# Kernel tuning notes

Measured on AMD Instinct MI355X. Metric: run time of the kernel, lower is better.

## Reference

```python
import jax, jax.numpy as jnp
import numpy as np

V = 50000
E = 300000
B = 4
LAT = 512
H = 128
L = 3


def setup_inputs() -> dict:
    key = jax.random.key(0)
    ks = jax.random.split(key, 8)
    vertex_xyz = jax.random.normal(ks[0], (V, 3), jnp.float32)
    latent = jax.random.normal(ks[1], (B, LAT), jnp.float32)
    edge_index = jax.random.randint(ks[2], (2, E), 0, V, dtype=jnp.int32)
    def lin(k, out_f, in_f):
        return jax.random.normal(k, (out_f, in_f), jnp.float32) / np.float32(np.sqrt(in_f))
    W_in = lin(ks[3], H, LAT + 3)
    b_in = jnp.zeros((H,), jnp.float32)
    conv_W = jax.random.normal(ks[4], (L, H, H), jnp.float32) / np.float32(np.sqrt(H))
    conv_b = jnp.zeros((L, H), jnp.float32)
    W_out = lin(ks[5], 3, H)
    b_out = jnp.zeros((3,), jnp.float32)
    return dict(vertex_xyz=vertex_xyz, latent=latent, edge_index=edge_index,
                W_in=W_in, b_in=b_in, conv_W=conv_W, conv_b=conv_b,
                W_out=W_out, b_out=b_out)


def _edge_norm(edge_index, B_, V_):
    """GCN symmetric normalization for edge_index tiled B times (same node ids,
    as in the original code's edge_index.repeat(1, B)) plus self-loops on all
    N = B*V flattened nodes. Structure is identical across layers, so compute once."""
    N = B_ * V_
    ei = jnp.tile(edge_index, (1, B_))                 # (2, E*B), ids in [0, V)
    loops = jnp.arange(N, dtype=edge_index.dtype)
    row = jnp.concatenate([ei[0], loops])              # source
    col = jnp.concatenate([ei[1], loops])              # target
    deg = jax.ops.segment_sum(jnp.ones(row.shape, jnp.float32), col, num_segments=N)
    dis = jnp.where(deg > 0, jax.lax.rsqrt(jnp.maximum(deg, 1.0)), 0.0)
    norm = dis[row] * dis[col]                         # (E*B + N,)
    return row, col, norm, N


def reference(vertex_xyz, latent, edge_index, W_in, b_in, conv_W, conv_b, W_out, b_out):
    B_, V_ = latent.shape[0], vertex_xyz.shape[0]
    row, col, norm, N = _edge_norm(edge_index, B_, V_)

    # concat template xyz with broadcast latent -> (B*V, LAT+3)
    x = jnp.concatenate([
        jnp.broadcast_to(vertex_xyz[None], (B_, V_, 3)),
        jnp.broadcast_to(latent[:, None, :], (B_, V_, latent.shape[-1])),
    ], axis=-1).reshape(B_ * V_, -1)

    x = jax.nn.relu(x @ W_in.T + b_in)                 # (N, H)

    for l in range(conv_W.shape[0]):
        h = x @ conv_W[l].T                            # linear (no bias before aggregation)
        agg = jax.ops.segment_sum(norm[:, None] * h[row], col, num_segments=N)
        x = jax.nn.relu(agg + conv_b[l])

    out = x @ W_out.T + b_out                          # (N, 3)
    return out.reshape(B_, V_, 3)
```

## Files before the change

### kernel.cpp

```cpp
#include <hip/hip_runtime.h>
#include <hip/hip_bf16.h>

typedef __attribute__((ext_vector_type(8))) short short8;
typedef __attribute__((ext_vector_type(4))) float f32x4;

#define V_ 50000
#define E_ 300000
#define B_ 4
#define LAT_ 512
#define H_ 128
#define L_ 3
#define N_ (B_*V_)

#define SCAN_B 512
#define SCAN_G ((V_ + SCAN_B - 1) / SCAN_B)

__device__ inline void bsplit(float v, ushort& hi, ushort& lo) {
    __hip_bfloat16 hb = __float2bfloat16(v);
    float hf = __bfloat162float(hb);
    __hip_bfloat16 lb = __float2bfloat16(v - hf);
    hi = *(ushort*)&hb; lo = *(ushort*)&lb;
}
__device__ inline float bjoin(ushort h, ushort l) {
    __hip_bfloat16 hb = *(__hip_bfloat16*)&h;
    __hip_bfloat16 lb = *(__hip_bfloat16*)&l;
    return __bfloat162float(hb) + __bfloat162float(lb);
}


__global__ void k_zero(int* __restrict__ deg, int* __restrict__ cursor) {
    int i = blockIdx.x * 256 + threadIdx.x;
    if (i < V_) { deg[i] = 0; cursor[i] = 0; }
}

__global__ void k_deg(const int* __restrict__ dst, int* __restrict__ deg) {
    int e = blockIdx.x * 256 + threadIdx.x;
    if (e < E_) atomicAdd(&deg[dst[e]], 1);
}

__global__ __launch_bounds__(SCAN_B) void k_scan1(const int* __restrict__ deg,
                                                  int* __restrict__ off,
                                                  float* __restrict__ dis,
                                                  int* __restrict__ part) {
    int t = threadIdx.x;
    int i = blockIdx.x * SCAN_B + t;
    int d = (i < V_) ? deg[i] : 0;
    __shared__ int sm[SCAN_B];
    sm[t] = d;
    __syncthreads();
    int val = d;
    for (int s = 1; s < SCAN_B; s <<= 1) {
        int o = (t >= s) ? sm[t - s] : 0;
        __syncthreads();
        val += o;
        sm[t] = val;
        __syncthreads();
    }
    if (i < V_) {
        off[i] = val - d;
        dis[i] = rsqrtf((float)(B_ * d + 1));
    }
    if (t == SCAN_B - 1) part[blockIdx.x] = val;
}

__global__ void k_scan2(int* __restrict__ part) {
    __shared__ int sm[128];
    int t = threadIdx.x;
    int v = (t < SCAN_G) ? part[t] : 0;
    sm[t] = v;
    __syncthreads();
    int val = v;
    for (int s = 1; s < 128; s <<= 1) {
        int o = (t >= s) ? sm[t - s] : 0;
        __syncthreads();
        val += o;
        sm[t] = val;
        __syncthreads();
    }
    if (t < SCAN_G) part[t] = val - v;
}

__global__ __launch_bounds__(SCAN_B) void k_scan3(int* __restrict__ off,
                                                  const int* __restrict__ part) {
    int i = blockIdx.x * SCAN_B + threadIdx.x;
    if (i < V_) off[i] += part[blockIdx.x];
    if (i == 0) off[V_] = E_;
}

__global__ void k_fill(const int* __restrict__ src, const int* __restrict__ dst,
                       const int* __restrict__ off, int* __restrict__ cursor,
                       int* __restrict__ csr) {
    int e = blockIdx.x * 256 + threadIdx.x;
    if (e < E_) {
        int c = dst[e];
        int p = atomicAdd(&cursor[c], 1);
        csr[off[c] + p] = src[e];
    }
}


__global__ void k_wsplit(const float* __restrict__ W, ushort* __restrict__ Whi,
                         ushort* __restrict__ Wlo) {
    int i = blockIdx.x * 256 + threadIdx.x;
    float w = W[i];
    ushort hi, lo; bsplit(w, hi, lo);
    Whi[i] = hi; Wlo[i] = lo;
}

__global__ void k_latproj(const float* __restrict__ Win, const float* __restrict__ bin,
                          const float* __restrict__ latent, float* __restrict__ latproj) {
    int t = blockIdx.x * 128 + threadIdx.x;
    if (t >= B_ * H_) return;
    int b = t >> 7, j = t & 127;
    const float* wr = Win + (size_t)j * (LAT_ + 3) + 3;
    const float* lp = latent + (size_t)b * LAT_;
    float s = bin[j];
    for (int k = 0; k < LAT_; k++) s = fmaf(wr[k], lp[k], s);
    latproj[t] = s;
}


__global__ __launch_bounds__(512, 4) void k_big(
        const float* __restrict__ xyz, const float* __restrict__ latproj,
        const float* __restrict__ Win,
        const ushort* __restrict__ Whi, const ushort* __restrict__ Wlo,
        const float* __restrict__ convb,
        const float* __restrict__ Wout, const float* __restrict__ bout,
        float* __restrict__ out) {
    __shared__ __align__(16) char smem[65536];
    const int tid = threadIdx.x;
    const int row0 = V_ + blockIdx.x * 64;
    const int lane = tid & 63;
    const int wid  = tid >> 6;
    const int l15  = lane & 15;
    const int kg   = lane >> 4;
    const int n0   = wid * 16;
    const int tr   = tid >> 4;
    const int c0   = (tid & 15) * 8;

#pragma unroll
    for (int rep = 0; rep < 2; rep++) {
        int row = tr + rep * 32;
        int node = row0 + row;
        ushort hs[8], ls[8];
        if (node < N_) {
            int v = node % V_, b = node / V_;
            float xv0 = xyz[v*3+0], xv1 = xyz[v*3+1], xv2 = xyz[v*3+2];
#pragma unroll
            for (int i = 0; i < 8; i++) {
                int j = c0 + i;
                float s = latproj[b*H_ + j];
                s = fmaf(Win[(size_t)j*(LAT_+3)+0], xv0, s);
                s = fmaf(Win[(size_t)j*(LAT_+3)+1], xv1, s);
                s = fmaf(Win[(size_t)j*(LAT_+3)+2], xv2, s);
                s = fmaxf(s, 0.f);
                bsplit(s, hs[i], ls[i]);
            }
        } else {
#pragma unroll
            for (int i = 0; i < 8; i++) { hs[i] = 0; ls[i] = 0; }
        }
        int bo = (c0*2) ^ ((row & 7) << 4);
        *(uint4*)(smem + row*256 + bo) = *(uint4*)hs;
        *(uint4*)(smem + 16384 + row*256 + bo) = *(uint4*)ls;
    }
    __syncthreads();

    int cur = 0;
    for (int l = 0; l < L_; l++) {
        const ushort* Whp = Whi + (size_t)l*H_*H_;
        const ushort* Wlp = Wlo + (size_t)l*H_*H_;
        short8 wh[4], wl[4];
#pragma unroll
        for (int ks = 0; ks < 4; ks++) {
            const ushort* bh = Whp + (size_t)(n0 + l15)*H_ + ks*32 + kg*4;
            const ushort* bl = Wlp + (size_t)(n0 + l15)*H_ + ks*32 + kg*4;
            union { short8 v; uint2 u[2]; } uh, ul;
            uh.u[0] = *(const uint2*)bh;  uh.u[1] = *(const uint2*)(bh + 16);
            ul.u[0] = *(const uint2*)bl;  ul.u[1] = *(const uint2*)(bl + 16);
            wh[ks] = uh.v; wl[ks] = ul.v;
        }
        const char* sb = smem + cur*32768;
        f32x4 acc[4];
#pragma unroll
        for (int mt = 0; mt < 4; mt++) acc[mt] = (f32x4){0.f,0.f,0.f,0.f};
#pragma unroll
        for (int mt = 0; mt < 4; mt++) {
            int row = mt*16 + l15;
            int swz = (row & 7) << 4;
            const char* rbh = sb + row*256;
            const char* rbl = sb + 16384 + row*256;
#pragma unroll
            for (int ks = 0; ks < 4; ks++) {
                int cc = ks*64 + kg*8;
                union { short8 v; uint2 u[2]; } ah, al;
                ah.u[0] = *(const uint2*)(rbh + (cc ^ swz));
                ah.u[1] = *(const uint2*)(rbh + ((cc+32) ^ swz));
                al.u[0] = *(const uint2*)(rbl + (cc ^ swz));
                al.u[1] = *(const uint2*)(rbl + ((cc+32) ^ swz));
                acc[mt] = __builtin_amdgcn_mfma_f32_16x16x32_bf16(ah.v, wh[ks], acc[mt], 0,0,0);
                acc[mt] = __builtin_amdgcn_mfma_f32_16x16x32_bf16(al.v, wh[ks], acc[mt], 0,0,0);
                acc[mt] = __builtin_amdgcn_mfma_f32_16x16x32_bf16(ah.v, wl[ks], acc[mt], 0,0,0);
            }
        }
        __syncthreads();
        char* db = smem + (cur^1)*32768;
        float bv = convb[l*H_ + n0 + l15];
        int bo = (n0 + l15) * 2;
#pragma unroll
        for (int mt = 0; mt < 4; mt++)
#pragma unroll
            for (int j = 0; j < 4; j++) {
                int row = mt*16 + kg*4 + j;
                int swz = (row & 7) << 4;
                float v = fmaxf(acc[mt][j] + bv, 0.f);
                ushort hi, lo; bsplit(v, hi, lo);
                *(ushort*)(db + row*256 + (bo ^ swz)) = hi;
                *(ushort*)(db + 16384 + row*256 + (bo ^ swz)) = lo;
            }
        __syncthreads();
        cur ^= 1;
    }

    const char* ob = smem + cur*32768;
    float wo0[8], wo1[8], wo2[8];
#pragma unroll
    for (int i = 0; i < 8; i++) {
        wo0[i] = Wout[0*H_ + c0 + i];
        wo1[i] = Wout[1*H_ + c0 + i];
        wo2[i] = Wout[2*H_ + c0 + i];
    }
#pragma unroll
    for (int rep = 0; rep < 2; rep++) {
        int row = tr + rep*32;
        int node = row0 + row;
        int bo = (c0*2) ^ ((row & 7) << 4);
        uint4 uh = *(const uint4*)(ob + row*256 + bo);
        uint4 ul = *(const uint4*)(ob + 16384 + row*256 + bo);
        const ushort* hp = (const ushort*)&uh;
        const ushort* lp = (const ushort*)&ul;
        float p0 = 0.f, p1 = 0.f, p2 = 0.f;
#pragma unroll
        for (int i = 0; i < 8; i++) {
            float xv = bjoin(hp[i], lp[i]);
            p0 = fmaf(xv, wo0[i], p0);
            p1 = fmaf(xv, wo1[i], p1);
            p2 = fmaf(xv, wo2[i], p2);
        }
#pragma unroll
        for (int m = 1; m < 16; m <<= 1) {
            p0 += __shfl_xor(p0, m);
            p1 += __shfl_xor(p1, m);
            p2 += __shfl_xor(p2, m);
        }
        if ((tid & 15) == 0 && node < N_) {
            out[(size_t)node*3 + 0] = p0 + bout[0];
            out[(size_t)node*3 + 1] = p1 + bout[1];
            out[(size_t)node*3 + 2] = p2 + bout[2];
        }
    }
}


template<int MODE>
__global__ __launch_bounds__(256, 4) void k_layerb0(
        const ushort* __restrict__ xh, const ushort* __restrict__ xl,
        const float* __restrict__ xyz, const float* __restrict__ latproj,
        const float* __restrict__ Win,
        const ushort* __restrict__ Whp, const ushort* __restrict__ Wlp,
        float* __restrict__ h) {
    __shared__ __align__(16) char smem[16896];
    const int tid = threadIdx.x;
    const int row0 = blockIdx.x * 32;
    const int lane = tid & 63;
    const int wid  = tid >> 6;
    const int l15  = lane & 15;
    const int kg   = lane >> 4;
    const int n0   = wid * 32;
    const int tr   = tid >> 4;
    const int c0   = (tid & 15) * 8;

    if (MODE == 0) {
#pragma unroll
        for (int rep = 0; rep < 2; rep++) {
            int row = tr + rep * 16;
            int v = row0 + row;
            ushort hs[8], ls[8];
            if (v < V_) {
                float xv0 = xyz[v*3+0], xv1 = xyz[v*3+1], xv2 = xyz[v*3+2];
#pragma unroll
                for (int i = 0; i < 8; i++) {
                    int j = c0 + i;
                    float s = latproj[j];
                    s = fmaf(Win[(size_t)j*(LAT_+3)+0], xv0, s);
                    s = fmaf(Win[(size_t)j*(LAT_+3)+1], xv1, s);
                    s = fmaf(Win[(size_t)j*(LAT_+3)+2], xv2, s);
                    s = fmaxf(s, 0.f);
                    bsplit(s, hs[i], ls[i]);
                }
            } else {
#pragma unroll
                for (int i = 0; i < 8; i++) { hs[i] = 0; ls[i] = 0; }
            }
            int bo = (c0*2) ^ ((row & 7) << 4);
            *(uint4*)(smem + row*256 + bo) = *(uint4*)hs;
            *(uint4*)(smem + 8192 + row*256 + bo) = *(uint4*)ls;
        }
    } else {
#pragma unroll
        for (int k = 0; k < 4; k++) {
            int chunk = tid + k*256;
            int p  = chunk >> 9;
            int r  = (chunk >> 4) & 31;
            int cb = (chunk & 15) * 16;
            int grow = row0 + r;
            uint4 g = {0u,0u,0u,0u};
            if (grow < V_)
                g = *(const uint4*)((const char*)((p ? xl : xh) + (size_t)grow*H_) + cb);
            *(uint4*)(smem + p*8192 + r*256 + (cb ^ ((r & 7) << 4))) = g;
        }
    }
    __syncthreads();

    short8 wh[2][4], wl[2][4];
#pragma unroll
    for (int nt = 0; nt < 2; nt++)
#pragma unroll
        for (int ks = 0; ks < 4; ks++) {
            const ushort* bh = Whp + (size_t)(n0 + nt*16 + l15)*H_ + ks*32 + kg*4;
            const ushort* bl = Wlp + (size_t)(n0 + nt*16 + l15)*H_ + ks*32 + kg*4;
            union { short8 v; uint2 u[2]; } uh, ul;
            uh.u[0] = *(const uint2*)bh;  uh.u[1] = *(const uint2*)(bh + 16);
            ul.u[0] = *(const uint2*)bl;  ul.u[1] = *(const uint2*)(bl + 16);
            wh[nt][ks] = uh.v; wl[nt][ks] = ul.v;
        }

    f32x4 acc[2][2];
#pragma unroll
    for (int mt = 0; mt < 2; mt++)
#pragma unroll
        for (int nt = 0; nt < 2; nt++) acc[mt][nt] = (f32x4){0.f,0.f,0.f,0.f};
#pragma unroll
    for (int mt = 0; mt < 2; mt++) {
        int row = mt*16 + l15;
        int swz = (row & 7) << 4;
        const char* rbh = smem + row*256;
        const char* rbl = smem + 8192 + row*256;
#pragma unroll
        for (int ks = 0; ks < 4; ks++) {
            int cc = ks*64 + kg*8;
            union { short8 v; uint2 u[2]; } ah, al;
            ah.u[0] = *(const uint2*)(rbh + (cc ^ swz));
            ah.u[1] = *(const uint2*)(rbh + ((cc+32) ^ swz));
            al.u[0] = *(const uint2*)(rbl + (cc ^ swz));
            al.u[1] = *(const uint2*)(rbl + ((cc+32) ^ swz));
#pragma unroll
            for (int nt = 0; nt < 2; nt++) {
                acc[mt][nt] = __builtin_amdgcn_mfma_f32_16x16x32_bf16(ah.v, wh[nt][ks], acc[mt][nt], 0,0,0);
                acc[mt][nt] = __builtin_amdgcn_mfma_f32_16x16x32_bf16(al.v, wh[nt][ks], acc[mt][nt], 0,0,0);
                acc[mt][nt] = __builtin_amdgcn_mfma_f32_16x16x32_bf16(ah.v, wl[nt][ks], acc[mt][nt], 0,0,0);
            }
        }
    }
    __syncthreads();

    float* bb = (float*)smem;
#pragma unroll
    for (int mt = 0; mt < 2; mt++)
#pragma unroll
        for (int nt = 0; nt < 2; nt++)
#pragma unroll
            for (int j = 0; j < 4; j++)
                bb[(mt*16 + kg*4 + j)*132 + n0 + nt*16 + l15] = acc[mt][nt][j];
    __syncthreads();

#pragma unroll
    for (int rep = 0; rep < 2; rep++) {
        int row = tr + rep*16;
        int grow = row0 + row;
        if (grow < V_) {
            f32x4 a = *(const f32x4*)&bb[row*132 + c0];
            f32x4 b = *(const f32x4*)&bb[row*132 + c0 + 4];
            *(f32x4*)(h + (size_t)grow*H_ + c0)     = a;
            *(f32x4*)(h + (size_t)grow*H_ + c0 + 4) = b;
        }
    }
}


template<bool FINAL>
__global__ __launch_bounds__(256) void k_agg0(const float* __restrict__ h,
                                              const float* __restrict__ dis,
                                              const int* __restrict__ off,
                                              const int* __restrict__ csr,
                                              const float* __restrict__ bias,
                                              ushort* __restrict__ xh_out,
                                              ushort* __restrict__ xl_out,
                                              const float* __restrict__ Wout,
                                              const float* __restrict__ bout,
                                              float* __restrict__ out) {
    int c = blockIdx.x * 4 + (threadIdx.x >> 6);
    int lane = threadIdx.x & 63;
    if (c >= V_) return;
    int beg = off[c], end = off[c + 1];
    int nu = end - beg;
    int   myu  = (lane < nu) ? csr[beg + lane] : 0;
    float mywu = (lane < nu) ? dis[myu] : 0.f;
    float a0 = 0.f, a1 = 0.f;
    int nn = nu < 64 ? nu : 64;
    for (int i = 0; i < nn; i++) {
        int u = __shfl(myu, i);
        float wu = __shfl(mywu, i);
        const float* hu = h + (size_t)u * 128;
        a0 = fmaf(wu, hu[lane],      a0);
        a1 = fmaf(wu, hu[lane + 64], a1);
    }
    for (int i = beg + 64; i < end; i++) {
        int u = csr[i];
        float wu = dis[u];
        const float* hu = h + (size_t)u * 128;
        a0 = fmaf(wu, hu[lane],      a0);
        a1 = fmaf(wu, hu[lane + 64], a1);
    }
    float dc = dis[c];
    const float* hr = h + (size_t)c * 128;
    float s0 = fmaxf(dc * (float)B_ * a0 + dc * dc * hr[lane]      + bias[lane],      0.f);
    float s1 = fmaxf(dc * (float)B_ * a1 + dc * dc * hr[lane + 64] + bias[lane + 64], 0.f);
    if (FINAL) {
        float p0 = s0 * Wout[0*H_ + lane] + s1 * Wout[0*H_ + 64 + lane];
        float p1 = s0 * Wout[1*H_ + lane] + s1 * Wout[1*H_ + 64 + lane];
        float p2 = s0 * Wout[2*H_ + lane] + s1 * Wout[2*H_ + 64 + lane];
#pragma unroll
        for (int d = 32; d; d >>= 1) {
            p0 += __shfl_down(p0, d);
            p1 += __shfl_down(p1, d);
            p2 += __shfl_down(p2, d);
        }
        if (lane == 0) {
            out[(size_t)c*3 + 0] = p0 + bout[0];
            out[(size_t)c*3 + 1] = p1 + bout[1];
            out[(size_t)c*3 + 2] = p2 + bout[2];
        }
    } else {
        ushort h0, l0, h1, l1;
        bsplit(s0, h0, l0);
        bsplit(s1, h1, l1);
        xh_out[(size_t)c*128 + lane]      = h0;
        xl_out[(size_t)c*128 + lane]      = l0;
        xh_out[(size_t)c*128 + lane + 64] = h1;
        xl_out[(size_t)c*128 + lane + 64] = l1;
    }
}


extern "C" void kernel_launch(void* const* d_in, const int* in_sizes, int n_in,
                              void* d_out, int out_size, void* d_ws, size_t ws_size,
                              hipStream_t stream) {
    const float* xyz    = (const float*)d_in[0];
    const float* latent = (const float*)d_in[1];
    const int*   ei     = (const int*)d_in[2];
    const float* Win    = (const float*)d_in[3];
    const float* bin    = (const float*)d_in[4];
    const float* convW  = (const float*)d_in[5];
    const float* convb  = (const float*)d_in[6];
    const float* Wout   = (const float*)d_in[7];
    const float* bout   = (const float*)d_in[8];
    float* out = (float*)d_out;

    char* w = (char*)d_ws;
    auto carve = [&](size_t bytes) {
        char* p = w;
        w += (bytes + 255) & ~(size_t)255;
        return p;
    };
    ushort* xh      = (ushort*)carve((size_t)V_ * H_ * 2);
    ushort* xl      = (ushort*)carve((size_t)V_ * H_ * 2);
    float*  h       = (float*)carve((size_t)V_ * H_ * 4);
    ushort* Whi     = (ushort*)carve((size_t)L_ * H_ * H_ * 2);
    ushort* Wlo     = (ushort*)carve((size_t)L_ * H_ * H_ * 2);
    float*  dis     = (float*)carve((size_t)V_ * 4);
    float*  latproj = (float*)carve((size_t)B_ * H_ * 4);
    int*    deg     = (int*)carve((size_t)V_ * 4);
    int*    off     = (int*)carve((size_t)(V_ + 1) * 4);
    int*    cursor  = (int*)carve((size_t)V_ * 4);
    int*    csr     = (int*)carve((size_t)E_ * 4);
    int*    part    = (int*)carve((size_t)SCAN_G * 4);
    (void)ws_size; (void)in_sizes; (void)n_in; (void)out_size;

    const int* src = ei;
    const int* dst = ei + E_;

    k_zero<<<(V_ + 255) / 256, 256, 0, stream>>>(deg, cursor);
    k_deg<<<(E_ + 255) / 256, 256, 0, stream>>>(dst, deg);
    k_scan1<<<SCAN_G, SCAN_B, 0, stream>>>(deg, off, dis, part);
    k_scan2<<<1, 128, 0, stream>>>(part);
    k_scan3<<<SCAN_G, SCAN_B, 0, stream>>>(off, part);
    k_fill<<<(E_ + 255) / 256, 256, 0, stream>>>(src, dst, off, cursor, csr);

    k_wsplit<<<(L_ * H_ * H_) / 256, 256, 0, stream>>>(convW, Whi, Wlo);
    k_latproj<<<4, 128, 0, stream>>>(Win, bin, latent, latproj);

    k_big<<<(N_ - V_ + 63) / 64, 512, 0, stream>>>(xyz, latproj, Win, Whi, Wlo,
                                                   convb, Wout, bout, out);

    const int GB0 = (V_ + 31) / 32;
    k_layerb0<0><<<GB0, 256, 0, stream>>>(nullptr, nullptr, xyz, latproj, Win,
                                          Whi, Wlo, h);
    k_agg0<false><<<(V_ + 3) / 4, 256, 0, stream>>>(h, dis, off, csr, convb,
                                                    xh, xl, nullptr, nullptr, nullptr);
    k_layerb0<1><<<GB0, 256, 0, stream>>>(xh, xl, nullptr, nullptr, nullptr,
                                          Whi + (size_t)1*H_*H_, Wlo + (size_t)1*H_*H_, h);
    k_agg0<false><<<(V_ + 3) / 4, 256, 0, stream>>>(h, dis, off, csr, convb + 1*H_,
                                                    xh, xl, nullptr, nullptr, nullptr);
    k_layerb0<1><<<GB0, 256, 0, stream>>>(xh, xl, nullptr, nullptr, nullptr,
                                          Whi + (size_t)2*H_*H_, Wlo + (size_t)2*H_*H_, h);
    k_agg0<true><<<(V_ + 3) / 4, 256, 0, stream>>>(h, dis, off, csr, convb + 2*H_,
                                                   nullptr, nullptr, Wout, bout, out);
}
```

Baseline: 436.3 us.

## Single-buffer k_big smem, widen layer GEMM tiles, repack xyz weights, improve swizzle

k_big drops its double-buffered 64KB LDS to a single 32KB buffer. The two existing barriers per layer already separate reads from writes, so this cuts LDS use per block. The V-row layer GEMM kernel moves to 64-row tiles with 512 threads and writes MFMA accumulators straight to global memory, removing the LDS transpose staging. The xyz columns of W_in are repacked once into a float4 array so each output needs one vector load instead of three strided loads. The swizzle also now XORs in bit 3 of the row to reduce LDS bank conflicts. The direct global stores are less coalesced than the old staged f32x4 stores, and the launch bounds change from (512,4) to (512,2), which may alter register allocation.

```diff
diff --git a/kernel.cpp b/kernel.cpp
--- a/kernel.cpp
+++ b/kernel.cpp
@@ -26,6 +26,7 @@
     __hip_bfloat16 lb = *(__hip_bfloat16*)&l;
     return __bfloat162float(hb) + __bfloat162float(lb);
 }
+__device__ inline int swzr(int row) { return ((row & 7) << 4) ^ ((row & 8) << 2); }
 
 
 __global__ void k_zero(int* __restrict__ deg, int* __restrict__ cursor) {
@@ -107,6 +108,13 @@
     Whi[i] = hi; Wlo[i] = lo;
 }
 
+__global__ void k_prep(const float* __restrict__ Win, float* __restrict__ Wxyz) {
+    int j = threadIdx.x;
+    f32x4 v = {Win[(size_t)j*(LAT_+3)+0], Win[(size_t)j*(LAT_+3)+1],
+               Win[(size_t)j*(LAT_+3)+2], 0.f};
+    *(f32x4*)(Wxyz + j*4) = v;
+}
+
 __global__ void k_latproj(const float* __restrict__ Win, const float* __restrict__ bin,
                           const float* __restrict__ latent, float* __restrict__ latproj) {
     int t = blockIdx.x * 128 + threadIdx.x;
@@ -120,14 +128,14 @@
 }
 
 
-__global__ __launch_bounds__(512, 4) void k_big(
+__global__ __launch_bounds__(512, 2) void k_big(
         const float* __restrict__ xyz, const float* __restrict__ latproj,
-        const float* __restrict__ Win,
+        const float* __restrict__ Wxyz,
         const ushort* __restrict__ Whi, const ushort* __restrict__ Wlo,
         const float* __restrict__ convb,
         const float* __restrict__ Wout, const float* __restrict__ bout,
         float* __restrict__ out) {
-    __shared__ __align__(16) char smem[65536];
+    __shared__ __align__(16) char smem[32768];
     const int tid = threadIdx.x;
     const int row0 = V_ + blockIdx.x * 64;
     const int lane = tid & 63;
@@ -149,10 +157,11 @@
 #pragma unroll
             for (int i = 0; i < 8; i++) {
                 int j = c0 + i;
+                f32x4 wx = *(const f32x4*)(Wxyz + j*4);
                 float s = latproj[b*H_ + j];
-                s = fmaf(Win[(size_t)j*(LAT_+3)+0], xv0, s);
-                s = fmaf(Win[(size_t)j*(LAT_+3)+1], xv1, s);
-                s = fmaf(Win[(size_t)j*(LAT_+3)+2], xv2, s);
+                s = fmaf(wx[0], xv0, s);
+                s = fmaf(wx[1], xv1, s);
+                s = fmaf(wx[2], xv2, s);
                 s = fmaxf(s, 0.f);
                 bsplit(s, hs[i], ls[i]);
             }
@@ -160,13 +169,12 @@
 #pragma unroll
             for (int i = 0; i < 8; i++) { hs[i] = 0; ls[i] = 0; }
         }
-        int bo = (c0*2) ^ ((row & 7) << 4);
+        int bo = (c0*2) ^ swzr(row);
         *(uint4*)(smem + row*256 + bo) = *(uint4*)hs;
         *(uint4*)(smem + 16384 + row*256 + bo) = *(uint4*)ls;
     }
     __syncthreads();
 
-    int cur = 0;
     for (int l = 0; l < L_; l++) {
         const ushort* Whp = Whi + (size_t)l*H_*H_;
         const ushort* Wlp = Wlo + (size_t)l*H_*H_;
@@ -180,31 +188,29 @@
             ul.u[0] = *(const uint2*)bl;  ul.u[1] = *(const uint2*)(bl + 16);
             wh[ks] = uh.v; wl[ks] = ul.v;
         }
-        const char* sb = smem + cur*32768;
         f32x4 acc[4];
 #pragma unroll
         for (int mt = 0; mt < 4; mt++) acc[mt] = (f32x4){0.f,0.f,0.f,0.f};
 #pragma unroll
         for (int mt = 0; mt < 4; mt++) {
             int row = mt*16 + l15;
-            int swz = (row & 7) << 4;
-            const char* rbh = sb + row*256;
-            const char* rbl = sb + 16384 + row*256;
+            int sw = swzr(row);
+            const char* rbh = smem + row*256;
+            const char* rbl = smem + 16384 + row*256;
 #pragma unroll
             for (int ks = 0; ks < 4; ks++) {
                 int cc = ks*64 + kg*8;
                 union { short8 v; uint2 u[2]; } ah, al;
-                ah.u[0] = *(const uint2*)(rbh + (cc ^ swz));
-                ah.u[1] = *(const uint2*)(rbh + ((cc+32) ^ swz));
-                al.u[0] = *(const uint2*)(rbl + (cc ^ swz));
-                al.u[1] = *(const uint2*)(rbl + ((cc+32) ^ swz));
+                ah.u[0] = *(const uint2*)(rbh + (cc ^ sw));
+                ah.u[1] = *(const uint2*)(rbh + ((cc+32) ^ sw));
+                al.u[0] = *(const uint2*)(rbl + (cc ^ sw));
+                al.u[1] = *(const uint2*)(rbl + ((cc+32) ^ sw));
                 acc[mt] = __builtin_amdgcn_mfma_f32_16x16x32_bf16(ah.v, wh[ks], acc[mt], 0,0,0);
                 acc[mt] = __builtin_amdgcn_mfma_f32_16x16x32_bf16(al.v, wh[ks], acc[mt], 0,0,0);
                 acc[mt] = __builtin_amdgcn_mfma_f32_16x16x32_bf16(ah.v, wl[ks], acc[mt], 0,0,0);
             }
         }
         __syncthreads();
-        char* db = smem + (cur^1)*32768;
         float bv = convb[l*H_ + n0 + l15];
         int bo = (n0 + l15) * 2;
 #pragma unroll
@@ -212,17 +218,15 @@
 #pragma unroll
             for (int j = 0; j < 4; j++) {
                 int row = mt*16 + kg*4 + j;
-                int swz = (row & 7) << 4;
+                int sw = swzr(row);
                 float v = fmaxf(acc[mt][j] + bv, 0.f);
                 ushort hi, lo; bsplit(v, hi, lo);
-                *(ushort*)(db + row*256 + (bo ^ swz)) = hi;
-                *(ushort*)(db + 16384 + row*256 + (bo ^ swz)) = lo;
+                *(ushort*)(smem + row*256 + (bo ^ sw)) = hi;
+                *(ushort*)(smem + 16384 + row*256 + (bo ^ sw)) = lo;
             }
         __syncthreads();
-        cur ^= 1;
-    }
-
-    const char* ob = smem + cur*32768;
+    }
+
     float wo0[8], wo1[8], wo2[8];
 #pragma unroll
     for (int i = 0; i < 8; i++) {
@@ -234,9 +238,9 @@
     for (int rep = 0; rep < 2; rep++) {
         int row = tr + rep*32;
         int node = row0 + row;
-        int bo = (c0*2) ^ ((row & 7) << 4);
-        uint4 uh = *(const uint4*)(ob + row*256 + bo);
-        uint4 ul = *(const uint4*)(ob + 16384 + row*256 + bo);
+        int bo = (c0*2) ^ swzr(row);
+        uint4 uh = *(const uint4*)(smem + row*256 + bo);
+        uint4 ul = *(const uint4*)(smem + 16384 + row*256 + bo);
         const ushort* hp = (const ushort*)&uh;
         const ushort* lp = (const ushort*)&ul;
         float p0 = 0.f, p1 = 0.f, p2 = 0.f;
@@ -263,27 +267,27 @@
 
 
 template<int MODE>
-__global__ __launch_bounds__(256, 4) void k_layerb0(
+__global__ __launch_bounds__(512, 2) void k_lay0(
         const ushort* __restrict__ xh, const ushort* __restrict__ xl,
         const float* __restrict__ xyz, const float* __restrict__ latproj,
-        const float* __restrict__ Win,
+        const float* __restrict__ Wxyz,
         const ushort* __restrict__ Whp, const ushort* __restrict__ Wlp,
         float* __restrict__ h) {
-    __shared__ __align__(16) char smem[16896];
+    __shared__ __align__(16) char smem[32768];
     const int tid = threadIdx.x;
-    const int row0 = blockIdx.x * 32;
+    const int row0 = blockIdx.x * 64;
     const int lane = tid & 63;
     const int wid  = tid >> 6;
     const int l15  = lane & 15;
     const int kg   = lane >> 4;
-    const int n0   = wid * 32;
+    const int n0   = wid * 16;
     const int tr   = tid >> 4;
     const int c0   = (tid & 15) * 8;
 
     if (MODE == 0) {
 #pragma unroll
         for (int rep = 0; rep < 2; rep++) {
-            int row = tr + rep * 16;
+            int row = tr + rep * 32;
             int v = row0 + row;
             ushort hs[8], ls[8];
             if (v < V_) {
@@ -291,10 +295,11 @@
 #pragma unroll
                 for (int i = 0; i < 8; i++) {
                     int j = c0 + i;
+                    f32x4 wx = *(const f32x4*)(Wxyz + j*4);
                     float s = latproj[j];
-                    s = fmaf(Win[(size_t)j*(LAT_+3)+0], xv0, s);
-                    s = fmaf(Win[(size_t)j*(LAT_+3)+1], xv1, s);
-                    s = fmaf(Win[(size_t)j*(LAT_+3)+2], xv2, s);
+                    s = fmaf(wx[0], xv0, s);
+                    s = fmaf(wx[1], xv1, s);
+                    s = fmaf(wx[2], xv2, s);
                     s = fmaxf(s, 0.f);
                     bsplit(s, hs[i], ls[i]);
                 }
@@ -302,89 +307,67 @@
 #pragma unroll
                 for (int i = 0; i < 8; i++) { hs[i] = 0; ls[i] = 0; }
             }
-            int bo = (c0*2) ^ ((row & 7) << 4);
+            int bo = (c0*2) ^ swzr(row);
             *(uint4*)(smem + row*256 + bo) = *(uint4*)hs;
-            *(uint4*)(smem + 8192 + row*256 + bo) = *(uint4*)ls;
+            *(uint4*)(smem + 16384 + row*256 + bo) = *(uint4*)ls;
         }
     } else {
 #pragma unroll
         for (int k = 0; k < 4; k++) {
-            int chunk = tid + k*256;
-            int p  = chunk >> 9;
-            int r  = (chunk >> 4) & 31;
+            int chunk = tid + k*512;
+            int p  = chunk >> 10;
+            int r  = (chunk >> 4) & 63;
             int cb = (chunk & 15) * 16;
             int grow = row0 + r;
             uint4 g = {0u,0u,0u,0u};
             if (grow < V_)
                 g = *(const uint4*)((const char*)((p ? xl : xh) + (size_t)grow*H_) + cb);
-            *(uint4*)(smem + p*8192 + r*256 + (cb ^ ((r & 7) << 4))) = g;
+            *(uint4*)(smem + p*16384 + r*256 + (cb ^ swzr(r))) = g;
         }
     }
     __syncthreads();
 
-    short8 wh[2][4], wl[2][4];
-#pragma unroll
-    for (int nt = 0; nt < 2; nt++)
-#pragma unroll
-        for (int ks = 0; ks < 4; ks++) {
-            const ushort* bh = Whp + (size_t)(n0 + nt*16 + l15)*H_ + ks*32 + kg*4;
-            const ushort* bl = Wlp + (size_t)(n0 + nt*16 + l15)*H_ + ks*32 + kg*4;
-            union { short8 v; uint2 u[2]; } uh, ul;
-            uh.u[0] = *(const uint2*)bh;  uh.u[1] = *(const uint2*)(bh + 16);
-            ul.u[0] = *(const uint2*)bl;  ul.u[1] = *(const uint2*)(bl + 16);
-            wh[nt][ks] = uh.v; wl[nt][ks] = ul.v;
-        }
-
-    f32x4 acc[2][2];
-#pragma unroll
-    for (int mt = 0; mt < 2; mt++)
-#pragma unroll
-        for (int nt = 0; nt < 2; nt++) acc[mt][nt] = (f32x4){0.f,0.f,0.f,0.f};
-#pragma unroll
-    for (int mt = 0; mt < 2; mt++) {
+    short8 wh[4], wl[4];
+#pragma unroll
+    for (int ks = 0; ks < 4; ks++) {
+        const ushort* bh = Whp + (size_t)(n0 + l15)*H_ + ks*32 + kg*4;
+        const ushort* bl = Wlp + (size_t)(n0 + l15)*H_ + ks*32 + kg*4;
+        union { short8 v; uint2 u[2]; } uh, ul;
+        uh.u[0] = *(const uint2*)bh;  uh.u[1] = *(const uint2*)(bh + 16);
+        ul.u[0] = *(const uint2*)bl;  ul.u[1] = *(const uint2*)(bl + 16);
+        wh[ks] = uh.v; wl[ks] = ul.v;
+    }
+
+    f32x4 acc[4];
+#pragma unroll
+    for (int mt = 0; mt < 4; mt++) acc[mt] = (f32x4){0.f,0.f,0.f,0.f};
+#pragma unroll
+    for (int mt = 0; mt < 4; mt++) {
         int row = mt*16 + l15;
-        int swz = (row & 7) << 4;
+        int sw = swzr(row);
         const char* rbh = smem + row*256;
-        const char* rbl = smem + 8192 + row*256;
+        const char* rbl = smem + 16384 + row*256;
 #pragma unroll
         for (int ks = 0; ks < 4; ks++) {
             int cc = ks*64 + kg*8;
             union { short8 v; uint2 u[2]; } ah, al;
-            ah.u[0] = *(const uint2*)(rbh + (cc ^ swz));
-            ah.u[1] = *(const uint2*)(rbh + ((cc+32) ^ swz));
-            al.u[0] = *(const uint2*)(rbl + (cc ^ swz));
-            al.u[1] = *(const uint2*)(rbl + ((cc+32) ^ swz));
-#pragma unroll
-            for (int nt = 0; nt < 2; nt++) {
-                acc[mt][nt] = __builtin_amdgcn_mfma_f32_16x16x32_bf16(ah.v, wh[nt][ks], acc[mt][nt], 0,0,0);
-                acc[mt][nt] = __builtin_amdgcn_mfma_f32_16x16x32_bf16(al.v, wh[nt][ks], acc[mt][nt], 0,0,0);
-                acc[mt][nt] = __builtin_amdgcn_mfma_f32_16x16x32_bf16(ah.v, wl[nt][ks], acc[mt][nt], 0,0,0);
-            }
-        }
-    }
-    __syncthreads();
-
-    float* bb = (float*)smem;
-#pragma unroll
-    for (int mt = 0; mt < 2; mt++)
-#pragma unroll
-        for (int nt = 0; nt < 2; nt++)
-#pragma unroll
-            for (int j = 0; j < 4; j++)
-                bb[(mt*16 + kg*4 + j)*132 + n0 + nt*16 + l15] = acc[mt][nt][j];
-    __syncthreads();
-
-#pragma unroll
-    for (int rep = 0; rep < 2; rep++) {
-        int row = tr + rep*16;
-        int grow = row0 + row;
-        if (grow < V_) {
-            f32x4 a = *(const f32x4*)&bb[row*132 + c0];
-            f32x4 b = *(const f32x4*)&bb[row*132 + c0 + 4];
-            *(f32x4*)(h + (size_t)grow*H_ + c0)     = a;
-            *(f32x4*)(h + (size_t)grow*H_ + c0 + 4) = b;
-        }
-    }
+            ah.u[0] = *(const uint2*)(rbh + (cc ^ sw));
+            ah.u[1] = *(const uint2*)(rbh + ((cc+32) ^ sw));
+            al.u[0] = *(const uint2*)(rbl + (cc ^ sw));
+            al.u[1] = *(const uint2*)(rbl + ((cc+32) ^ sw));
+            acc[mt] = __builtin_amdgcn_mfma_f32_16x16x32_bf16(ah.v, wh[ks], acc[mt], 0,0,0);
+            acc[mt] = __builtin_amdgcn_mfma_f32_16x16x32_bf16(al.v, wh[ks], acc[mt], 0,0,0);
+            acc[mt] = __builtin_amdgcn_mfma_f32_16x16x32_bf16(ah.v, wl[ks], acc[mt], 0,0,0);
+        }
+    }
+
+#pragma unroll
+    for (int mt = 0; mt < 4; mt++)
+#pragma unroll
+        for (int j = 0; j < 4; j++) {
+            int grow = row0 + mt*16 + kg*4 + j;
+            if (grow < V_) h[(size_t)grow*H_ + n0 + l15] = acc[mt][j];
+        }
 }
 
 
@@ -480,6 +463,7 @@
     ushort* Wlo     = (ushort*)carve((size_t)L_ * H_ * H_ * 2);
     float*  dis     = (float*)carve((size_t)V_ * 4);
     float*  latproj = (float*)carve((size_t)B_ * H_ * 4);
+    float*  Wxyz    = (float*)carve((size_t)H_ * 4 * 4);
     int*    deg     = (int*)carve((size_t)V_ * 4);
     int*    off     = (int*)carve((size_t)(V_ + 1) * 4);
     int*    cursor  = (int*)carve((size_t)V_ * 4);
@@ -498,22 +482,23 @@
     k_fill<<<(E_ + 255) / 256, 256, 0, stream>>>(src, dst, off, cursor, csr);
 
     k_wsplit<<<(L_ * H_ * H_) / 256, 256, 0, stream>>>(convW, Whi, Wlo);
+    k_prep<<<1, 128, 0, stream>>>(Win, Wxyz);
     k_latproj<<<4, 128, 0, stream>>>(Win, bin, latent, latproj);
 
-    k_big<<<(N_ - V_ + 63) / 64, 512, 0, stream>>>(xyz, latproj, Win, Whi, Wlo,
+    k_big<<<(N_ - V_ + 63) / 64, 512, 0, stream>>>(xyz, latproj, Wxyz, Whi, Wlo,
                                                    convb, Wout, bout, out);
 
-    const int GB0 = (V_ + 31) / 32;
-    k_layerb0<0><<<GB0, 256, 0, stream>>>(nullptr, nullptr, xyz, latproj, Win,
-                                          Whi, Wlo, h);
+    const int GB0 = (V_ + 63) / 64;
+    k_lay0<0><<<GB0, 512, 0, stream>>>(nullptr, nullptr, xyz, latproj, Wxyz,
+                                       Whi, Wlo, h);
     k_agg0<false><<<(V_ + 3) / 4, 256, 0, stream>>>(h, dis, off, csr, convb,
                                                     xh, xl, nullptr, nullptr, nullptr);
-    k_layerb0<1><<<GB0, 256, 0, stream>>>(xh, xl, nullptr, nullptr, nullptr,
-                                          Whi + (size_t)1*H_*H_, Wlo + (size_t)1*H_*H_, h);
+    k_lay0<1><<<GB0, 512, 0, stream>>>(xh, xl, nullptr, nullptr, nullptr,
+                                       Whi + (size_t)1*H_*H_, Wlo + (size_t)1*H_*H_, h);
     k_agg0<false><<<(V_ + 3) / 4, 256, 0, stream>>>(h, dis, off, csr, convb + 1*H_,
                                                     xh, xl, nullptr, nullptr, nullptr);
-    k_layerb0<1><<<GB0, 256, 0, stream>>>(xh, xl, nullptr, nullptr, nullptr,
-                                          Whi + (size_t)2*H_*H_, Wlo + (size_t)2*H_*H_, h);
+    k_lay0<1><<<GB0, 512, 0, stream>>>(xh, xl, nullptr, nullptr, nullptr,
+                                       Whi + (size_t)2*H_*H_, Wlo + (size_t)2*H_*H_, h);
     k_agg0<true><<<(V_ + 3) / 4, 256, 0, stream>>>(h, dis, off, csr, convb + 2*H_,
                                                    nullptr, nullptr, Wout, bout, out);
 }
```

Result: faster. 416.1 us (-4.6%).
